# Performance work log

Measured on AMD Instinct MI355X. Metric: run time of the kernel, lower is better.

Reference implementation:

```python
import jax, jax.numpy as jnp
import numpy as np

GAMMA = 0.1   # sdtw_gamma from train_config
WARP = 1.0    # sdtw_warp from train_config
BIG = 1e8     # stand-in for +inf in the DP table (safe in fp32 logsumexp)


def soft_dtw(D, gamma, warp):
    """SoftDTW with warp penalty via anti-diagonal wavefront DP.

    D: [B, N, M] pairwise cost matrix. Returns [B] soft-DTW values.
    Recurrence: R[i,j] = D[i,j] + softmin_gamma(R[i-1,j-1], R[i-1,j]+warp, R[i,j-1]+warp)
    """
    B, N, M = D.shape
    R = jnp.full((B, N + 1, M + 1), BIG, D.dtype)
    R = R.at[:, 0, 0].set(0.0)
    ii = jnp.arange(N)  # cell row indices on a diagonal

    def body(R, k):
        jj = k - ii                       # cell col indices, i+j = k
        valid = (jj >= 0) & (jj < M)
        jc = jnp.clip(jj, 0, M - 1)
        # padded-coordinate predecessors of cell (ii, jj)
        r_diag = R[:, ii, jc]             # R[i-1, j-1]
        r_up = R[:, ii, jc + 1] + warp    # R[i-1, j] + warp
        r_left = R[:, ii + 1, jc] + warp  # R[i, j-1] + warp
        stacked = jnp.stack([r_diag, r_up, r_left], axis=0)  # [3, B, N]
        smin = -gamma * jax.nn.logsumexp(-stacked / gamma, axis=0)
        new = D[:, ii, jc] + smin
        cur = R[:, ii + 1, jc + 1]
        upd = jnp.where(valid[None, :], new, cur)
        # row indices ii+1 are all distinct -> no scatter collisions
        R = R.at[:, ii + 1, jc + 1].set(upd)
        return R, None

    R, _ = jax.lax.scan(body, R, jnp.arange(N + M - 1))
    return R[:, N, M]


def setup_inputs() -> dict:
    key = jax.random.key(0)
    k1, k2, k3, k4 = jax.random.split(key, 4)
    mel_pred = jax.random.normal(k1, (4, 512, 80), dtype=jnp.float32)
    mel_target = jax.random.normal(k2, (4, 512, 80), dtype=jnp.float32)
    log_d_pred = jax.random.normal(k3, (4, 128), dtype=jnp.float32)
    d_target = jax.random.randint(k4, (4, 128), 0, 20)
    return {"mel_pred": mel_pred, "mel_target": mel_target,
            "log_d_pred": log_d_pred, "d_target": d_target}


def reference(mel_pred, mel_target, log_d_pred, d_target):
    B, T, _ = mel_pred.shape
    # pairwise L1 frame distance: D[b,i,j] = sum_m |pred[b,i,m] - tgt[b,j,m]|
    D = jnp.abs(mel_pred[:, :, None, :] - mel_target[:, None, :, :]).sum(-1)
    sdtw = soft_dtw(D, GAMMA, WARP)           # [B]
    mel_loss = (sdtw / T).mean()
    # L1 (reduction='none' -> mean) on log-durations
    log_d_target = jnp.log(d_target.astype(jnp.float32) + 1.0)
    duration_loss = jnp.abs(log_d_pred - log_d_target).mean()
    return mel_loss + duration_loss
```

## Files before the change

### kernel.cpp

```cpp
#include <hip/hip_runtime.h>
#include <hip/hip_bf16.h>
#include <math.h>

#define BIGF 1e8f

__device__ inline float min3f(float a, float b, float c) {
    float d;
    asm("v_min3_f32 %0, %1, %2, %3" : "=v"(d) : "v"(a), "v"(b), "v"(c));
    return d;
}

__global__ __launch_bounds__(256) void prep_kernel(
        const float* __restrict__ pred, const float* __restrict__ targ,
        float* __restrict__ Ddiag) {
    const int bid = blockIdx.x;
    const int t   = threadIdx.x;

    if (bid < 256) {
        const int b  = bid >> 6;
        const int i0 = ((bid >> 3) & 7) * 64;
        const int j0 = (bid & 7) * 64;
        __shared__ float sp[64][81];
        __shared__ float st[64][81];

        const float4* __restrict__ p4 = (const float4*)(pred + ((size_t)b * 512 + i0) * 80);
        const float4* __restrict__ t4 = (const float4*)(targ + ((size_t)b * 512 + j0) * 80);
        #pragma unroll
        for (int q = 0; q < 5; ++q) {
            int idx = q * 256 + t;
            int r = idx / 20, dq = idx % 20;
            float4 v = p4[r * 20 + dq];
            sp[r][dq*4+0]=v.x; sp[r][dq*4+1]=v.y; sp[r][dq*4+2]=v.z; sp[r][dq*4+3]=v.w;
            float4 w = t4[r * 20 + dq];
            st[r][dq*4+0]=w.x; st[r][dq*4+1]=w.y; st[r][dq*4+2]=w.z; st[r][dq*4+3]=w.w;
        }
        __syncthreads();

        const int tx = t & 15, ty = t >> 4;
        float acc[4][4];
        #pragma unroll
        for (int r = 0; r < 4; ++r)
            #pragma unroll
            for (int c = 0; c < 4; ++c) acc[r][c] = 0.f;

        #pragma unroll 4
        for (int d = 0; d < 80; ++d) {
            float a0 = sp[4*ty+0][d], a1 = sp[4*ty+1][d], a2 = sp[4*ty+2][d], a3 = sp[4*ty+3][d];
            float b0 = st[4*tx+0][d], b1 = st[4*tx+1][d], b2 = st[4*tx+2][d], b3 = st[4*tx+3][d];
            acc[0][0] += fabsf(a0-b0); acc[0][1] += fabsf(a0-b1); acc[0][2] += fabsf(a0-b2); acc[0][3] += fabsf(a0-b3);
            acc[1][0] += fabsf(a1-b0); acc[1][1] += fabsf(a1-b1); acc[1][2] += fabsf(a1-b2); acc[1][3] += fabsf(a1-b3);
            acc[2][0] += fabsf(a2-b0); acc[2][1] += fabsf(a2-b1); acc[2][2] += fabsf(a2-b2); acc[2][3] += fabsf(a2-b3);
            acc[3][0] += fabsf(a3-b0); acc[3][1] += fabsf(a3-b1); acc[3][2] += fabsf(a3-b2); acc[3][3] += fabsf(a3-b3);
        }

        #pragma unroll
        for (int r = 0; r < 4; ++r) {
            #pragma unroll
            for (int c = 0; c < 4; ++c) {
                int i = i0 + 4*ty + r;
                int j = j0 + 4*tx + c;
                float v = acc[r][c];
                v = ((i | j) == 0) ? (v - BIGF) : (v + 2.0f);
                Ddiag[((size_t)b * 1023 + (i + j)) * 512 + i] = v;
            }
        }
    } else {
        unsigned fid  = bid - 256;
        unsigned base = fid * 2048u + (unsigned)t * 8u;
        #pragma unroll
        for (int e = 0; e < 8; ++e) {
            unsigned slot = base + e;
            unsigned rem  = slot % 523776u;
            int k = (int)(rem >> 9);
            int i = (int)(rem & 511u);
            int j = k - i;
            if ((unsigned)j >= 512u) Ddiag[slot] = BIGF;
        }
    }
}

#define STEP(V1, V2, da, db)                                                  \
  {                                                                           \
    float nb1 = __int_as_float(__builtin_amdgcn_update_dpp(                   \
        __float_as_int(BIGF), __float_as_int(V1[7]), 0x138, 0xF, 0xF, false));\
    float nb2 = __int_as_float(__builtin_amdgcn_update_dpp(                   \
        __float_as_int(BIGF), __float_as_int(V2[7]), 0x138, 0xF, 0xF, false));\
    V2[7] = db.w + min3f(V2[6], V1[6], V1[7]);                                \
    V2[6] = db.z + min3f(V2[5], V1[5], V1[6]);                                \
    V2[5] = db.y + min3f(V2[4], V1[4], V1[5]);                                \
    V2[4] = db.x + min3f(V2[3], V1[3], V1[4]);                                \
    V2[3] = da.w + min3f(V2[2], V1[2], V1[3]);                                \
    V2[2] = da.z + min3f(V2[1], V1[1], V1[2]);                                \
    V2[1] = da.y + min3f(V2[0], V1[0], V1[1]);                                \
    V2[0] = da.x + min3f(nb2,   nb1,   V1[0]);                                \
  }

__global__ __launch_bounds__(64, 1) void dp_kernel(
        const float* __restrict__ Ddiag, float* __restrict__ sdtw) {
    const int b    = blockIdx.x;
    const int lane = threadIdx.x;
    const char* __restrict__ base = (const char*)Ddiag + (size_t)b * (1023ull * 512 * 4);
    const unsigned loff = (unsigned)lane * 32u;

    float A[8], B[8];
    #pragma unroll
    for (int r = 0; r < 8; ++r) { A[r] = BIGF; B[r] = BIGF; }

    float4 Pa[16], Pb[16];
    #pragma unroll
    for (int p = 0; p < 16; ++p) {
        const char* s = base + (size_t)p * 2048 + loff;
        Pa[p] = *(const float4*)(s);
        Pb[p] = *(const float4*)(s + 16);
    }

    int k0 = 0;
    for (int t = 0; t < 63; ++t, k0 += 16) {
#define PH(p, Vx, Vy)                                                         \
        STEP(Vx, Vy, Pa[p], Pb[p])                                            \
        {                                                                     \
            int kp = k0 + 16 + (p); kp = (kp > 1022) ? 1022 : kp;             \
            const char* s = base + (size_t)kp * 2048 + loff;                  \
            Pa[p] = *(const float4*)(s);                                      \
            Pb[p] = *(const float4*)(s + 16);                                 \
        }
        PH(0,A,B)  PH(1,B,A)  PH(2,A,B)  PH(3,B,A)
        PH(4,A,B)  PH(5,B,A)  PH(6,A,B)  PH(7,B,A)
        PH(8,A,B)  PH(9,B,A)  PH(10,A,B) PH(11,B,A)
        PH(12,A,B) PH(13,B,A) PH(14,A,B) PH(15,B,A)
#undef PH
    }
    STEP(A,B,Pa[0],Pb[0])   STEP(B,A,Pa[1],Pb[1])   STEP(A,B,Pa[2],Pb[2])
    STEP(B,A,Pa[3],Pb[3])   STEP(A,B,Pa[4],Pb[4])   STEP(B,A,Pa[5],Pb[5])
    STEP(A,B,Pa[6],Pb[6])   STEP(B,A,Pa[7],Pb[7])   STEP(A,B,Pa[8],Pb[8])
    STEP(B,A,Pa[9],Pb[9])   STEP(A,B,Pa[10],Pb[10]) STEP(B,A,Pa[11],Pb[11])
    STEP(A,B,Pa[12],Pb[12]) STEP(B,A,Pa[13],Pb[13]) STEP(A,B,Pa[14],Pb[14])

    if (lane == 63) sdtw[b] = B[7] - 1022.0f;
}

__global__ __launch_bounds__(512) void finalize_kernel(
        const float* __restrict__ ldp, const int* __restrict__ dt,
        const float* __restrict__ sdtw, float* __restrict__ out) {
    const int t = threadIdx.x;
    float v = fabsf(ldp[t] - logf((float)dt[t] + 1.0f));
    #pragma unroll
    for (int o = 32; o > 0; o >>= 1) v += __shfl_down(v, o);
    __shared__ float part[8];
    if ((t & 63) == 0) part[t >> 6] = v;
    __syncthreads();
    if (t == 0) {
        float dur = 0.f;
        #pragma unroll
        for (int w = 0; w < 8; ++w) dur += part[w];
        dur *= (1.0f / 512.0f);
        float mel = (sdtw[0] + sdtw[1] + sdtw[2] + sdtw[3]) * (1.0f / (4.0f * 512.0f));
        out[0] = mel + dur;
    }
}

extern "C" void kernel_launch(void* const* d_in, const int* in_sizes, int n_in,
                              void* d_out, int out_size, void* d_ws, size_t ws_size,
                              hipStream_t stream) {
    const float* pred = (const float*)d_in[0];
    const float* targ = (const float*)d_in[1];
    const float* ldp  = (const float*)d_in[2];
    const int*   dt   = (const int*)d_in[3];
    float* out = (float*)d_out;

    float* Ddiag = (float*)d_ws;
    float* sdtw  = Ddiag + (size_t)4 * 1023 * 512;

    prep_kernel<<<256 + 1023, 256, 0, stream>>>(pred, targ, Ddiag);
    dp_kernel<<<4, 64, 0, stream>>>(Ddiag, sdtw);
    finalize_kernel<<<1, 512, 0, stream>>>(ldp, dt, sdtw, out);
}
```

Before: 80.01 us.

## Store diagonal cost matrix in fp16 and fold finalize into DP kernel

The anti-diagonal cost buffer is now stored as fp16 instead of fp32, which halves the bytes written by the prep kernel and streamed by the serial DP wavefront. The first cell is handled separately in registers, so no huge negative offset is needed. Out-of-band cells are padded with a large finite fp16 value, and the padding pass now runs per diagonal row instead of over every slot. The separate finalize kernel is removed: extra threads in block 0 compute the duration loss, and both partial losses are accumulated into the output with atomics after a memset. Rounding to fp16 adds precision error to the distances, and the floating-point atomic adds make the summation order nondeterministic.

Measured after the change: 77.95 us. 1.03x faster.

```diff
diff --git a/kernel.cpp b/kernel.cpp
--- a/kernel.cpp
+++ b/kernel.cpp
@@ -1,8 +1,10 @@
 #include <hip/hip_runtime.h>
 #include <hip/hip_bf16.h>
+#include <hip/hip_fp16.h>
 #include <math.h>
 
 #define BIGF 1e8f
+#define BIGS 28672.0f
 
 __device__ inline float min3f(float a, float b, float c) {
     float d;
@@ -12,7 +14,7 @@
 
 __global__ __launch_bounds__(256) void prep_kernel(
         const float* __restrict__ pred, const float* __restrict__ targ,
-        float* __restrict__ Ddiag) {
+        __half* __restrict__ Dh) {
     const int bid = blockIdx.x;
     const int t   = threadIdx.x;
 
@@ -60,103 +62,106 @@
                 int i = i0 + 4*ty + r;
                 int j = j0 + 4*tx + c;
                 float v = acc[r][c];
-                v = ((i | j) == 0) ? (v - BIGF) : (v + 2.0f);
-                Ddiag[((size_t)b * 1023 + (i + j)) * 512 + i] = v;
+                float w = ((i | j) == 0) ? v : (v + 2.0f);
+                Dh[((size_t)b * 1023 + (i + j)) * 512 + i] = __float2half(w);
             }
         }
     } else {
-        unsigned fid  = bid - 256;
-        unsigned base = fid * 2048u + (unsigned)t * 8u;
+        const int k  = bid - 256;
+        const int lo = (k > 511) ? (k - 511) : 0;
+        const int hi = (k < 511) ? k : 511;
+        const __half big = __float2half(BIGS);
         #pragma unroll
-        for (int e = 0; e < 8; ++e) {
-            unsigned slot = base + e;
-            unsigned rem  = slot % 523776u;
-            int k = (int)(rem >> 9);
-            int i = (int)(rem & 511u);
-            int j = k - i;
-            if ((unsigned)j >= 512u) Ddiag[slot] = BIGF;
+        for (int b = 0; b < 4; ++b) {
+            __half* row = Dh + ((size_t)b * 1023 + k) * 512;
+            int i1 = t;
+            int i2 = t + 256;
+            if (i1 < lo || i1 > hi) row[i1] = big;
+            if (i2 < lo || i2 > hi) row[i2] = big;
         }
     }
 }
 
-#define STEP(V1, V2, da, db)                                                  \
+#define DPPSHR(x) __int_as_float(__builtin_amdgcn_update_dpp(                 \
+        __float_as_int(BIGF), __float_as_int(x), 0x138, 0xF, 0xF, false))
+
+#define STEP(V1, V2, P)                                                       \
   {                                                                           \
-    float nb1 = __int_as_float(__builtin_amdgcn_update_dpp(                   \
-        __float_as_int(BIGF), __float_as_int(V1[7]), 0x138, 0xF, 0xF, false));\
-    float nb2 = __int_as_float(__builtin_amdgcn_update_dpp(                   \
-        __float_as_int(BIGF), __float_as_int(V2[7]), 0x138, 0xF, 0xF, false));\
-    V2[7] = db.w + min3f(V2[6], V1[6], V1[7]);                                \
-    V2[6] = db.z + min3f(V2[5], V1[5], V1[6]);                                \
-    V2[5] = db.y + min3f(V2[4], V1[4], V1[5]);                                \
-    V2[4] = db.x + min3f(V2[3], V1[3], V1[4]);                                \
-    V2[3] = da.w + min3f(V2[2], V1[2], V1[3]);                                \
-    V2[2] = da.z + min3f(V2[1], V1[1], V1[2]);                                \
-    V2[1] = da.y + min3f(V2[0], V1[0], V1[1]);                                \
-    V2[0] = da.x + min3f(nb2,   nb1,   V1[0]);                                \
+    const __half2* hp_ = (const __half2*)&(P);                                \
+    float2 f0_ = __half22float2(hp_[0]);                                      \
+    float2 f1_ = __half22float2(hp_[1]);                                      \
+    float2 f2_ = __half22float2(hp_[2]);                                      \
+    float2 f3_ = __half22float2(hp_[3]);                                      \
+    float nb1 = DPPSHR(V1[7]);                                                \
+    float nb2 = DPPSHR(V2[7]);                                                \
+    V2[7] = f3_.y + min3f(V2[6], V1[6], V1[7]);                               \
+    V2[6] = f3_.x + min3f(V2[5], V1[5], V1[6]);                               \
+    V2[5] = f2_.y + min3f(V2[4], V1[4], V1[5]);                               \
+    V2[4] = f2_.x + min3f(V2[3], V1[3], V1[4]);                               \
+    V2[3] = f1_.y + min3f(V2[2], V1[2], V1[3]);                               \
+    V2[2] = f1_.x + min3f(V2[1], V1[1], V1[2]);                               \
+    V2[1] = f0_.y + min3f(V2[0], V1[0], V1[1]);                               \
+    V2[0] = f0_.x + min3f(nb2,   nb1,   V1[0]);                               \
   }
 
-__global__ __launch_bounds__(64, 1) void dp_kernel(
-        const float* __restrict__ Ddiag, float* __restrict__ sdtw) {
+__global__ __launch_bounds__(128, 1) void dp_kernel(
+        const __half* __restrict__ Dh,
+        const float* __restrict__ ldp, const int* __restrict__ dt,
+        float* __restrict__ out) {
+    const int tid = threadIdx.x;
+    if (tid >= 64) {
+        if (blockIdx.x == 0) {
+            const int l = tid - 64;
+            float s = 0.f;
+            #pragma unroll
+            for (int q = 0; q < 8; ++q) {
+                int idx = l * 8 + q;
+                s += fabsf(ldp[idx] - logf((float)dt[idx] + 1.0f));
+            }
+            #pragma unroll
+            for (int o = 32; o > 0; o >>= 1) s += __shfl_down(s, o);
+            if (l == 0) atomicAdd(out, s * (1.0f / 512.0f));
+        }
+        return;
+    }
+
     const int b    = blockIdx.x;
-    const int lane = threadIdx.x;
-    const char* __restrict__ base = (const char*)Ddiag + (size_t)b * (1023ull * 512 * 4);
-    const unsigned loff = (unsigned)lane * 32u;
+    const int lane = tid;
+    const char* __restrict__ base = (const char*)(Dh + (size_t)b * 1023 * 512);
+    const unsigned loff = (unsigned)lane * 16u;
 
     float A[8], B[8];
     #pragma unroll
     for (int r = 0; r < 8; ++r) { A[r] = BIGF; B[r] = BIGF; }
 
-    float4 Pa[16], Pb[16];
-    #pragma unroll
-    for (int p = 0; p < 16; ++p) {
-        const char* s = base + (size_t)p * 2048 + loff;
-        Pa[p] = *(const float4*)(s);
-        Pb[p] = *(const float4*)(s + 16);
+    {
+        uint4 q0 = *(const uint4*)(base + loff);
+        float c00 = __half2float(*(const __half*)&q0.x);
+        B[0] = (lane == 0) ? c00 : BIGF;
     }
 
-    int k0 = 0;
+    uint4 P[16];
+    #pragma unroll
+    for (int p = 0; p < 16; ++p)
+        P[p] = *(const uint4*)(base + (size_t)(1 + p) * 1024 + loff);
+
+    int k0 = 1;
     for (int t = 0; t < 63; ++t, k0 += 16) {
 #define PH(p, Vx, Vy)                                                         \
-        STEP(Vx, Vy, Pa[p], Pb[p])                                            \
-        {                                                                     \
-            int kp = k0 + 16 + (p); kp = (kp > 1022) ? 1022 : kp;             \
-            const char* s = base + (size_t)kp * 2048 + loff;                  \
-            Pa[p] = *(const float4*)(s);                                      \
-            Pb[p] = *(const float4*)(s + 16);                                 \
-        }
-        PH(0,A,B)  PH(1,B,A)  PH(2,A,B)  PH(3,B,A)
-        PH(4,A,B)  PH(5,B,A)  PH(6,A,B)  PH(7,B,A)
-        PH(8,A,B)  PH(9,B,A)  PH(10,A,B) PH(11,B,A)
-        PH(12,A,B) PH(13,B,A) PH(14,A,B) PH(15,B,A)
+        STEP(Vx, Vy, P[p])                                                    \
+        P[p] = *(const uint4*)(base + (size_t)(k0 + 16 + p) * 1024 + loff);
+        PH(0,B,A)  PH(1,A,B)  PH(2,B,A)  PH(3,A,B)
+        PH(4,B,A)  PH(5,A,B)  PH(6,B,A)  PH(7,A,B)
+        PH(8,B,A)  PH(9,A,B)  PH(10,B,A) PH(11,A,B)
+        PH(12,B,A) PH(13,A,B) PH(14,B,A) PH(15,A,B)
 #undef PH
     }
-    STEP(A,B,Pa[0],Pb[0])   STEP(B,A,Pa[1],Pb[1])   STEP(A,B,Pa[2],Pb[2])
-    STEP(B,A,Pa[3],Pb[3])   STEP(A,B,Pa[4],Pb[4])   STEP(B,A,Pa[5],Pb[5])
-    STEP(A,B,Pa[6],Pb[6])   STEP(B,A,Pa[7],Pb[7])   STEP(A,B,Pa[8],Pb[8])
-    STEP(B,A,Pa[9],Pb[9])   STEP(A,B,Pa[10],Pb[10]) STEP(B,A,Pa[11],Pb[11])
-    STEP(A,B,Pa[12],Pb[12]) STEP(B,A,Pa[13],Pb[13]) STEP(A,B,Pa[14],Pb[14])
+    STEP(B,A,P[0])  STEP(A,B,P[1])  STEP(B,A,P[2])  STEP(A,B,P[3])
+    STEP(B,A,P[4])  STEP(A,B,P[5])  STEP(B,A,P[6])  STEP(A,B,P[7])
+    STEP(B,A,P[8])  STEP(A,B,P[9])  STEP(B,A,P[10]) STEP(A,B,P[11])
+    STEP(B,A,P[12]) STEP(A,B,P[13])
 
-    if (lane == 63) sdtw[b] = B[7] - 1022.0f;
-}
-
-__global__ __launch_bounds__(512) void finalize_kernel(
-        const float* __restrict__ ldp, const int* __restrict__ dt,
-        const float* __restrict__ sdtw, float* __restrict__ out) {
-    const int t = threadIdx.x;
-    float v = fabsf(ldp[t] - logf((float)dt[t] + 1.0f));
-    #pragma unroll
-    for (int o = 32; o > 0; o >>= 1) v += __shfl_down(v, o);
-    __shared__ float part[8];
-    if ((t & 63) == 0) part[t >> 6] = v;
-    __syncthreads();
-    if (t == 0) {
-        float dur = 0.f;
-        #pragma unroll
-        for (int w = 0; w < 8; ++w) dur += part[w];
-        dur *= (1.0f / 512.0f);
-        float mel = (sdtw[0] + sdtw[1] + sdtw[2] + sdtw[3]) * (1.0f / (4.0f * 512.0f));
-        out[0] = mel + dur;
-    }
+    if (lane == 63) atomicAdd(out, (B[7] - 1022.0f) * (1.0f / 2048.0f));
 }
 
 extern "C" void kernel_launch(void* const* d_in, const int* in_sizes, int n_in,
@@ -168,10 +173,9 @@
     const int*   dt   = (const int*)d_in[3];
     float* out = (float*)d_out;
 
-    float* Ddiag = (float*)d_ws;
-    float* sdtw  = Ddiag + (size_t)4 * 1023 * 512;
+    __half* Dh = (__half*)d_ws;
 
-    prep_kernel<<<256 + 1023, 256, 0, stream>>>(pred, targ, Ddiag);
-    dp_kernel<<<4, 64, 0, stream>>>(Ddiag, sdtw);
-    finalize_kernel<<<1, 512, 0, stream>>>(ldp, dt, sdtw, out);
+    hipMemsetAsync(out, 0, sizeof(float), stream);
+    prep_kernel<<<256 + 1023, 256, 0, stream>>>(pred, targ, Dh);
+    dp_kernel<<<4, 128, 0, stream>>>(Dh, ldp, dt, out);
 }
```
